# Kernel optimization log

Measured on AMD Instinct MI355X. Metric: run time of the kernel, lower is better.

## Reference

```python
import jax, jax.numpy as jnp
import numpy as np

SHIFT = 1  # fixed value of the randomized shift_direction (+1)


def setup_inputs() -> dict:
    key = jax.random.key(0)
    kx, kw = jax.random.split(key)
    x = jax.random.normal(kx, (1, 128, 56, 56), dtype=jnp.float32)
    W = jax.random.normal(kw, (32, 64, 3), dtype=jnp.float32)
    return {"x": x, "W": W}


def reference(x, W):
    # channel-pair sum: (1,128,56,56) -> (1,2,64,56,56) -> sum over pair axis
    t2 = x.reshape(1, 2, 64, 56, 56).sum(axis=1)  # (1,64,56,56)
    # unfold with kernel (3,1), padding (1,0): 3-tap window along H
    xp = jnp.pad(t2, ((0, 0), (0, 0), (1, 1), (0, 0)))  # (1,64,58,56)
    # t3[l,c,k,h,w] = xp[l,c,h+k,w]
    t3 = jnp.stack([xp[:, :, k:k + 56, :] for k in range(3)], axis=2)  # (1,64,3,56,56)
    # conv-as-einsum: contract channel and tap dims with weights (32,64,3)
    out = jnp.einsum('lckhw,ick->lihw', t3, W)  # (1,32,56,56)
    # roll shift along width (dim 3)
    return jnp.roll(out, SHIFT, axis=3)
```

## Files before the change

kernel.cpp:

```cpp
#include <hip/hip_runtime.h>

#define HW 56
#define PLANE 3136
#define CH 64
#define CI 32
#define NI 2

__global__ __launch_bounds__(256) void convshift_kernel(
    const float* __restrict__ x, const float* __restrict__ Wt, float* __restrict__ out)
{
    __shared__ float sW[NI * CH * 3];
    const int i0  = blockIdx.y * NI;
    const int tid = threadIdx.x;
    #pragma unroll
    for (int t = tid; t < NI * CH * 3; t += 256)
        sW[t] = Wt[i0 * (CH * 3) + t];
    __syncthreads();

    const int p  = blockIdx.x * 256 + tid;
    const int pc = (p < PLANE) ? p : (PLANE - 1);
    const int h  = pc / HW;
    const int w  = pc - h * HW;

    const bool v0 = (h > 0), v2 = (h < HW - 1);
    const int hm = v0 ? h - 1 : 0;
    const int hp = v2 ? h + 1 : HW - 1;

    const float* __restrict__ xa = x + w;
    const float* __restrict__ xb = x + CH * PLANE + w;
    const int r0 = hm * HW, r1 = h * HW, r2 = hp * HW;

    float acc[NI][3];
    #pragma unroll
    for (int ii = 0; ii < NI; ++ii) { acc[ii][0] = 0.f; acc[ii][1] = 0.f; acc[ii][2] = 0.f; }

    float A0[2][8], A1[2][8], A2[2][8], B0[2][8], B1[2][8], B2[2][8];

    #pragma unroll
    for (int j = 0; j < 8; ++j) {
        const int o = j * PLANE;
        A0[0][j] = xa[o + r0]; A1[0][j] = xa[o + r1]; A2[0][j] = xa[o + r2];
        B0[0][j] = xb[o + r0]; B1[0][j] = xb[o + r1]; B2[0][j] = xb[o + r2];
    }

    #pragma unroll
    for (int ch = 0; ch < 8; ++ch) {
        const int cur = ch & 1, nxt = cur ^ 1;
        if (ch < 7) {
            #pragma unroll
            for (int j = 0; j < 8; ++j) {
                const int o = ((ch + 1) * 8 + j) * PLANE;
                A0[nxt][j] = xa[o + r0]; A1[nxt][j] = xa[o + r1]; A2[nxt][j] = xa[o + r2];
                B0[nxt][j] = xb[o + r0]; B1[nxt][j] = xb[o + r1]; B2[nxt][j] = xb[o + r2];
            }
        }
        #pragma unroll
        for (int j = 0; j < 8; ++j) {
            const int c = ch * 8 + j;
            const float s0 = A0[cur][j] + B0[cur][j];
            const float s1 = A1[cur][j] + B1[cur][j];
            const float s2 = A2[cur][j] + B2[cur][j];
            #pragma unroll
            for (int ii = 0; ii < NI; ++ii) {
                acc[ii][0] += s0 * sW[ii * (CH * 3) + c * 3 + 0];
                acc[ii][1] += s1 * sW[ii * (CH * 3) + c * 3 + 1];
                acc[ii][2] += s2 * sW[ii * (CH * 3) + c * 3 + 2];
            }
        }
    }

    if (p < PLANE) {
        int wst = w + 1; if (wst == HW) wst = 0;
        #pragma unroll
        for (int ii = 0; ii < NI; ++ii) {
            float r = acc[ii][1];
            if (v0) r += acc[ii][0];
            if (v2) r += acc[ii][2];
            out[(i0 + ii) * PLANE + h * HW + wst] = r;
        }
    }
}

extern "C" void kernel_launch(void* const* d_in, const int* in_sizes, int n_in,
                              void* d_out, int out_size, void* d_ws, size_t ws_size,
                              hipStream_t stream) {
    const float* x  = (const float*)d_in[0];
    const float* Wt = (const float*)d_in[1];
    float* out = (float*)d_out;

    dim3 grid(13, CI / NI), block(256);
    hipLaunchKernelGGL(convshift_kernel, grid, block, 0, stream, x, Wt, out);
}
```

Measured before the change: 12.01 us.

## Split channel reduction across four wavefronts per block with shared-memory reduce

Each block now covers 64 pixels instead of 256, and its four wavefronts each take a quarter of the 64 input channels. Partial sums are combined through shared memory before the shifted store. The grid grows from 13 to 49 blocks per output pair, which raises parallelism and shortens each thread's serial load chain. The cost is an extra barrier and shared-memory reduction, plus fewer loads in flight per thread for hiding latency.

```diff
diff --git a/kernel.cpp b/kernel.cpp
--- a/kernel.cpp
+++ b/kernel.cpp
@@ -5,11 +5,15 @@
 #define CH 64
 #define CI 32
 #define NI 2
+#define NQ 4
+#define CQ (CH/NQ)
 
 __global__ __launch_bounds__(256) void convshift_kernel(
     const float* __restrict__ x, const float* __restrict__ Wt, float* __restrict__ out)
 {
     __shared__ float sW[NI * CH * 3];
+    __shared__ float red[NQ][NI][64];
+
     const int i0  = blockIdx.y * NI;
     const int tid = threadIdx.x;
     #pragma unroll
@@ -17,17 +21,19 @@
         sW[t] = Wt[i0 * (CH * 3) + t];
     __syncthreads();
 
-    const int p  = blockIdx.x * 256 + tid;
-    const int pc = (p < PLANE) ? p : (PLANE - 1);
-    const int h  = pc / HW;
-    const int w  = pc - h * HW;
+    const int px = tid & 63;
+    const int q  = tid >> 6;
+    const int p  = blockIdx.x * 64 + px;
+    const int h  = p / HW;
+    const int w  = p - h * HW;
 
     const bool v0 = (h > 0), v2 = (h < HW - 1);
     const int hm = v0 ? h - 1 : 0;
     const int hp = v2 ? h + 1 : HW - 1;
 
-    const float* __restrict__ xa = x + w;
-    const float* __restrict__ xb = x + CH * PLANE + w;
+    const int c0 = q * CQ;
+    const float* __restrict__ xa = x + c0 * PLANE + w;
+    const float* __restrict__ xb = x + (CH + c0) * PLANE + w;
     const int r0 = hm * HW, r1 = h * HW, r2 = hp * HW;
 
     float acc[NI][3];
@@ -44,40 +50,50 @@
     }
 
     #pragma unroll
-    for (int ch = 0; ch < 8; ++ch) {
-        const int cur = ch & 1, nxt = cur ^ 1;
-        if (ch < 7) {
+    for (int chk = 0; chk < 2; ++chk) {
+        const int cur = chk & 1, nxt = cur ^ 1;
+        if (chk < 1) {
             #pragma unroll
             for (int j = 0; j < 8; ++j) {
-                const int o = ((ch + 1) * 8 + j) * PLANE;
+                const int o = (8 + j) * PLANE;
                 A0[nxt][j] = xa[o + r0]; A1[nxt][j] = xa[o + r1]; A2[nxt][j] = xa[o + r2];
                 B0[nxt][j] = xb[o + r0]; B1[nxt][j] = xb[o + r1]; B2[nxt][j] = xb[o + r2];
             }
         }
         #pragma unroll
         for (int j = 0; j < 8; ++j) {
-            const int c = ch * 8 + j;
+            const int ca = c0 + chk * 8 + j;
             const float s0 = A0[cur][j] + B0[cur][j];
             const float s1 = A1[cur][j] + B1[cur][j];
             const float s2 = A2[cur][j] + B2[cur][j];
             #pragma unroll
             for (int ii = 0; ii < NI; ++ii) {
-                acc[ii][0] += s0 * sW[ii * (CH * 3) + c * 3 + 0];
-                acc[ii][1] += s1 * sW[ii * (CH * 3) + c * 3 + 1];
-                acc[ii][2] += s2 * sW[ii * (CH * 3) + c * 3 + 2];
+                acc[ii][0] += s0 * sW[ii * (CH * 3) + ca * 3 + 0];
+                acc[ii][1] += s1 * sW[ii * (CH * 3) + ca * 3 + 1];
+                acc[ii][2] += s2 * sW[ii * (CH * 3) + ca * 3 + 2];
             }
         }
     }
 
-    if (p < PLANE) {
-        int wst = w + 1; if (wst == HW) wst = 0;
-        #pragma unroll
-        for (int ii = 0; ii < NI; ++ii) {
-            float r = acc[ii][1];
-            if (v0) r += acc[ii][0];
-            if (v2) r += acc[ii][2];
-            out[(i0 + ii) * PLANE + h * HW + wst] = r;
-        }
+    #pragma unroll
+    for (int ii = 0; ii < NI; ++ii) {
+        float r = acc[ii][1];
+        if (v0) r += acc[ii][0];
+        if (v2) r += acc[ii][2];
+        red[q][ii][px] = r;
+    }
+    __syncthreads();
+
+    if (tid < NI * 64) {
+        const int ii  = tid >> 6;
+        const int px2 = tid & 63;
+        const float s = (red[0][ii][px2] + red[1][ii][px2])
+                      + (red[2][ii][px2] + red[3][ii][px2]);
+        const int p2 = blockIdx.x * 64 + px2;
+        const int h2 = p2 / HW;
+        const int w2 = p2 - h2 * HW;
+        int wst = w2 + 1; if (wst == HW) wst = 0;
+        out[(i0 + ii) * PLANE + h2 * HW + wst] = s;
     }
 }
 
@@ -88,6 +104,6 @@
     const float* Wt = (const float*)d_in[1];
     float* out = (float*)d_out;
 
-    dim3 grid(13, CI / NI), block(256);
+    dim3 grid(49, CI / NI), block(256);
     hipLaunchKernelGGL(convshift_kernel, grid, block, 0, stream, x, Wt, out);
 }
```

After: 10.34 us (median of 2 runs). -14.0%, faster.
